# Kernel tuning notes

Hardware: AMD Instinct MI355X
Metric: run time of the kernel (lower is better)

## Reference

```python
import jax, jax.numpy as jnp
import numpy as np

N = 2048       # num nodes
E = 4096       # num edges
D_NODE = 128
D_EDGE = 128
H = 4          # heads
DH = D_EDGE // H
C = 16         # num classes
NODE_K = N // 2   # node_k_ratio = 0.5
EDGE_K = E // 2   # edge_k_ratio = 0.5
NEG = -1e9


def setup_inputs() -> dict:
    key = jax.random.key(0)
    ks = jax.random.split(key, 16)
    w = lambda k, shape: jax.random.normal(k, shape, jnp.float32) * 0.02
    return {
        "node_features": jax.random.normal(ks[0], (N, D_NODE), jnp.float32),
        "edge_features": jax.random.normal(ks[1], (E, D_EDGE), jnp.float32),
        "edge_index": jax.random.randint(ks[2], (2, E), 0, N, jnp.int32),
        # ImportanceRouter: scalar scores per node / edge
        "w_router_n": w(ks[3], (D_NODE,)),
        "w_router_e": w(ks[4], (D_EDGE,)),
        # EdgeAttention projections
        "w_e": w(ks[5], (D_EDGE, D_EDGE)),
        "w_n": w(ks[6], (D_NODE, D_EDGE)),
        "w_q": w(ks[7], (D_EDGE, D_EDGE)),
        "w_k": w(ks[8], (D_EDGE, D_EDGE)),
        "w_v": w(ks[9], (D_EDGE, D_EDGE)),
        "w_o": w(ks[10], (D_EDGE, D_EDGE)),
        # classifier MLP: Linear -> GELU -> Linear
        "w1": w(ks[11], (D_EDGE, D_EDGE)),
        "b1": jnp.zeros((D_EDGE,), jnp.float32),
        "w2": w(ks[12], (D_EDGE, C)),
        "b2": jnp.zeros((C,), jnp.float32),
    }


def reference(node_features, edge_features, edge_index,
              w_router_n, w_router_e,
              w_e, w_n, w_q, w_k, w_v, w_o,
              w1, b1, w2, b2):
    src, dst = edge_index[0], edge_index[1]

    # --- ImportanceRouter: node/edge scores ---
    ns = node_features @ w_router_n   # [N]
    es = edge_features @ w_router_e   # [E]

    # --- apply_top_k(node_k_ratio=0.5, edge_k_ratio=0.5) ---
    _, nidx = jax.lax.top_k(ns, NODE_K)
    node_mask = jnp.zeros((N,), bool).at[nidx].set(True)
    _, eidx = jax.lax.top_k(es, EDGE_K)
    edge_topk = jnp.zeros((E,), bool).at[eidx].set(True)
    edge_mask = edge_topk & node_mask[src] & node_mask[dst]   # [E]

    ef = edge_features * edge_mask[:, None].astype(edge_features.dtype)

    # --- build_edge_adjacency: edges sharing a node attend to each other ---
    adj = ((src[:, None] == src[None, :]) | (src[:, None] == dst[None, :]) |
           (dst[:, None] == src[None, :]) | (dst[:, None] == dst[None, :]))  # [E,E]

    # --- EdgeAttention: edge rep mixes edge feats and endpoint node feats ---
    h = ef @ w_e + (node_features[src] + node_features[dst]) @ w_n   # [E, D_EDGE]
    q = (h @ w_q).reshape(E, H, DH)
    k = (h @ w_k).reshape(E, H, DH)
    v = (h @ w_v).reshape(E, H, DH)
    scores = jnp.einsum('ehd,fhd->hef', q, k) / np.float32(np.sqrt(DH))  # [H,E,E]
    scores = jnp.where(adj[None, :, :], scores, NEG)
    attn = jax.nn.softmax(scores, axis=-1)
    o = jnp.einsum('hef,fhd->ehd', attn, v).reshape(E, D_EDGE) @ w_o    # [E, D_EDGE]

    # --- classifier: Linear -> GELU -> Linear ---
    x = jax.nn.gelu(o @ w1 + b1)
    logits = x @ w2 + b2            # [E, C]
    return logits
```

## Files before the change

### kernel.cpp

```cpp
#include <hip/hip_runtime.h>
#include <hip/hip_bf16.h>
#include <math.h>

#define NN 2048
#define NE 4096
#define D 128
#define NODE_K 1024
#define EDGE_K 2048
#define CAP 64

typedef const __hip_bfloat16* bfp;
typedef unsigned short u16;
typedef __attribute__((ext_vector_type(8))) short short8;
typedef __attribute__((ext_vector_type(4))) float floatx4;

#define MFMA16(a, b, c) __builtin_amdgcn_mfma_f32_16x16x32_bf16(a, b, c, 0, 0, 0)

__device__ __forceinline__ float b2f(__hip_bfloat16 x) { return __bfloat162float(x); }

__device__ __forceinline__ float ldx(const void* p, size_t i, int f) {
  return f ? ((const float*)p)[i] : b2f(((bfp)p)[i]);
}
__device__ __forceinline__ float4 ldx4(const void* p, size_t i4, int f) {
  if (f) return ((const float4*)p)[i4];
  ushort4 u = ((const ushort4*)p)[i4];
  float4 r;
  r.x = __uint_as_float(((unsigned)u.x) << 16);
  r.y = __uint_as_float(((unsigned)u.y) << 16);
  r.z = __uint_as_float(((unsigned)u.z) << 16);
  r.w = __uint_as_float(((unsigned)u.w) << 16);
  return r;
}

__device__ __forceinline__ void split2(float x, u16& hi, u16& lo) {
  unsigned u = __float_as_uint(x);
  unsigned h = (u + 0x7FFFu + ((u >> 16) & 1u)) >> 16;
  hi = (u16)h;
  float r = x - __uint_as_float(h << 16);
  unsigned v = __float_as_uint(r);
  lo = (u16)((v + 0x7FFFu + ((v >> 16) & 1u)) >> 16);
}
__device__ __forceinline__ void build_frags(const float* v8, short8& fh, short8& fl) {
  #pragma unroll
  for (int i = 0; i < 8; ++i) {
    u16 h, l;
    split2(v8[i], h, l);
    fh[i] = (short)h; fl[i] = (short)l;
  }
}

__device__ __forceinline__ int detect_f(const u16* raw, int* s4) {
  int t = threadIdx.x;
  int weird = 0;
  for (int i = t; i < 1024; i += blockDim.x) {
    unsigned int bits = ((unsigned int)raw[i]) << 16;
    float x = __uint_as_float(bits);
    float ax = fabsf(x);
    if (!(ax <= 1e3f) || (x != 0.f && ax < 1e-12f)) weird++;
  }
  #pragma unroll
  for (int m = 32; m >= 1; m >>= 1) weird += __shfl_xor(weird, m);
  int nw = (int)blockDim.x >> 6;
  if ((t & 63) == 0) s4[t >> 6] = weird;
  __syncthreads();
  int tot = 0;
  for (int i = 0; i < nw; ++i) tot += s4[i];
  return (tot > 50) ? 1 : 0;
}

struct K1Args {
  const void *nf, *ef, *wrn, *wre;
  const void* w[7];
  float *ns, *es;
  int *deg, *flag;
  u16 *wtHi, *wtLo;
  u16 *feHi, *feLo;
};

#define SCORE_BLOCKS ((NN + NE) / 4)
#define WPREP_BLOCKS 112
#define FSPLIT_BLOCKS 192
__global__ __launch_bounds__(256) void scores_prep_kernel(K1Args a) {
  __shared__ int s4[4];
  int b = blockIdx.x, t = threadIdx.x;
  int f = detect_f((const u16*)a.nf, s4);
  if (b < SCORE_BLOCKS) {
    int wid = b * 4 + (t >> 6), lane = t & 63;
    const void* base; const void* w; float* out; size_t r0;
    if (wid < NN) { base = a.nf; r0 = (size_t)wid * D; w = a.wrn; out = a.ns + wid; }
    else { int r = wid - NN; base = a.ef; r0 = (size_t)r * D; w = a.wre; out = a.es + r; }
    double p = (double)ldx(base, r0 + lane, f) * (double)ldx(w, lane, f)
             + (double)ldx(base, r0 + lane + 64, f) * (double)ldx(w, lane + 64, f);
    #pragma unroll
    for (int m = 32; m >= 1; m >>= 1) p += __shfl_xor(p, m);
    if (lane == 0) *out = (float)p;
  } else if (b == SCORE_BLOCKS) {
    if (t == 0) a.flag[0] = f;
    for (int i = t; i < NN; i += 256) a.deg[i] = 0;
  } else if (b <= SCORE_BLOCKS + WPREP_BLOCKS) {
    int tau = (b - SCORE_BLOCKS - 1) * 256 + t;
    int w = tau >> 12, rem = tau & 4095;
    int n = rem >> 5, k0 = (rem & 31) * 4;
    ushort4 hi, lo;
    split2(ldx(a.w[w], (size_t)(k0 + 0) * 128 + n, f), hi.x, lo.x);
    split2(ldx(a.w[w], (size_t)(k0 + 1) * 128 + n, f), hi.y, lo.y);
    split2(ldx(a.w[w], (size_t)(k0 + 2) * 128 + n, f), hi.z, lo.z);
    split2(ldx(a.w[w], (size_t)(k0 + 3) * 128 + n, f), hi.w, lo.w);
    ((ushort4*)a.wtHi)[tau] = hi;
    ((ushort4*)a.wtLo)[tau] = lo;
  } else {
    int fb = b - SCORE_BLOCKS - 1 - WPREP_BLOCKS;
    #pragma unroll
    for (int i = 0; i < 4; ++i) {
      int g4 = fb * 1024 + i * 256 + t;
      float4 x = (g4 < NN * D / 4) ? ldx4(a.nf, g4, f)
                                   : ldx4(a.ef, g4 - NN * D / 4, f);
      ushort4 hi, lo;
      split2(x.x, hi.x, lo.x);
      split2(x.y, hi.y, lo.y);
      split2(x.z, hi.z, lo.z);
      split2(x.w, hi.w, lo.w);
      ((ushort4*)a.feHi)[g4] = hi;
      ((ushort4*)a.feLo)[g4] = lo;
    }
  }
}

#define NMB (NN / 4)
#define EMB (NE / 4)
__global__ __launch_bounds__(256) void mask_lists_kernel(
    const float* __restrict__ ns, const float* __restrict__ es,
    const int* __restrict__ src, const int* __restrict__ dst,
    int* __restrict__ node_mask, int* __restrict__ edge_topk,
    int* __restrict__ deg, int* __restrict__ lists) {
  __shared__ float s[NE];
  int b = blockIdx.x, t = threadIdx.x;
  if (b < NMB) {
    for (int i = t; i < NN; i += 256) s[i] = ns[i];
    __syncthreads();
    int i = b * 4 + (t >> 6), lane = t & 63;
    float si = s[i];
    int rank = 0;
    for (int j = lane; j < NN; j += 64) {
      float sj = s[j];
      rank += (sj > si) || (sj == si && j < i);
    }
    #pragma unroll
    for (int m = 32; m >= 1; m >>= 1) rank += __shfl_xor(rank, m);
    if (lane == 0) node_mask[i] = (rank < NODE_K) ? 1 : 0;
  } else if (b < NMB + EMB) {
    for (int i = t; i < NE; i += 256) s[i] = es[i];
    __syncthreads();
    int i = (b - NMB) * 4 + (t >> 6), lane = t & 63;
    float si = s[i];
    int rank = 0;
    for (int j = lane; j < NE; j += 64) {
      float sj = s[j];
      rank += (sj > si) || (sj == si && j < i);
    }
    #pragma unroll
    for (int m = 32; m >= 1; m >>= 1) rank += __shfl_xor(rank, m);
    if (lane == 0) edge_topk[i] = (rank < EDGE_K) ? 1 : 0;
  } else {
    int e = (b - NMB - EMB) * 256 + t;
    if (e < NE) {
      int sn = src[e], dn = dst[e];
      int p = atomicAdd(&deg[sn], 1);
      if (p >= 0 && p < CAP) lists[sn * CAP + p] = e;
      if (dn != sn) {
        p = atomicAdd(&deg[dn], 1);
        if (p >= 0 && p < CAP) lists[dn * CAP + p] = e;
      }
    }
  }
}

__global__ __launch_bounds__(512) void h_qkv_mfma_kernel(
    const u16* __restrict__ feHi, const u16* __restrict__ feLo,
    const int* __restrict__ src, const int* __restrict__ dst,
    const int* __restrict__ node_mask, const int* __restrict__ edge_topk,
    const u16* __restrict__ wtHi, const u16* __restrict__ wtLo,
    float* __restrict__ qkv) {
  __shared__ __align__(16) float hf[8 * 64 * 4];
  int t = threadIdx.x;
  int wave = t >> 6, lane = t & 63;
  int qd = lane >> 4, c = lane & 15;
  int row0 = blockIdx.x * 16;
  int e = row0 + c;
  int sn = src[e], dn = dst[e];
  bool em = edge_topk[e] && node_mask[sn] && node_mask[dn];
  int n0 = wave * 16;
  const u16* efH = feHi + (size_t)NN * D;
  const u16* efL = feLo + (size_t)NN * D;
  const short8 z8 = {0, 0, 0, 0, 0, 0, 0, 0};

  short8 A1h[4], A1l[4], Sh[4], Sl[4], Dh[4], Dl[4];
  short8 BEh[4], BEl[4], BNh[4], BNl[4];
  #pragma unroll
  for (int ks = 0; ks < 4; ++ks) {
    int k0 = ks * 32 + qd * 8;
    A1h[ks] = *(const short8*)(efH + (size_t)e * D + k0);
    A1l[ks] = *(const short8*)(efL + (size_t)e * D + k0);
    Sh[ks]  = *(const short8*)(feHi + (size_t)sn * D + k0);
    Sl[ks]  = *(const short8*)(feLo + (size_t)sn * D + k0);
    Dh[ks]  = *(const short8*)(feHi + (size_t)dn * D + k0);
    Dl[ks]  = *(const short8*)(feLo + (size_t)dn * D + k0);
    size_t bo = (size_t)(n0 + c) * 128 + k0;
    BEh[ks] = *(const short8*)(wtHi + bo);
    BEl[ks] = *(const short8*)(wtLo + bo);
    BNh[ks] = *(const short8*)(wtHi + 16384 + bo);
    BNl[ks] = *(const short8*)(wtLo + 16384 + bo);
  }
  if (!em) {
    #pragma unroll
    for (int ks = 0; ks < 4; ++ks) { A1h[ks] = z8; A1l[ks] = z8; }
  }
  floatx4 accE = {0.f, 0.f, 0.f, 0.f};
  floatx4 accN = {0.f, 0.f, 0.f, 0.f};
  #pragma unroll
  for (int ks = 0; ks < 4; ++ks) {
    accE = MFMA16(A1h[ks], BEh[ks], accE);
    accN = MFMA16(Sh[ks], BNh[ks], accN);
    accE = MFMA16(A1l[ks], BEh[ks], accE);
    accN = MFMA16(Sl[ks], BNh[ks], accN);
    accE = MFMA16(A1h[ks], BEl[ks], accE);
    accN = MFMA16(Sh[ks], BNl[ks], accN);
    accN = MFMA16(Dh[ks], BNh[ks], accN);
    accN = MFMA16(Dl[ks], BNh[ks], accN);
    accN = MFMA16(Dh[ks], BNl[ks], accN);
  }
  {
    int np = n0 + c;
    int kd = np >> 5, qq = (np >> 3) & 3, half = (c >> 2) & 1, j4 = c & 3;
    #pragma unroll
    for (int r = 0; r < 4; ++r)
      hf[((kd * 2 + half) * 64 + qq * 16 + 4 * qd + r) * 4 + j4] = accE[r] + accN[r];
  }
  short8 BQh[4], BQl[4], BKh[4], BKl[4], BVh[4], BVl[4];
  #pragma unroll
  for (int ks = 0; ks < 4; ++ks) {
    size_t bo = (size_t)(n0 + c) * 128 + ks * 32 + qd * 8;
    BQh[ks] = *(const short8*)(wtHi + 2 * 16384 + bo);
    BQl[ks] = *(const short8*)(wtLo + 2 * 16384 + bo);
    BKh[ks] = *(const short8*)(wtHi + 3 * 16384 + bo);
    BKl[ks] = *(const short8*)(wtLo + 3 * 16384 + bo);
    BVh[ks] = *(const short8*)(wtHi + 4 * 16384 + bo);
    BVl[ks] = *(const short8*)(wtLo + 4 * 16384 + bo);
  }
  __syncthreads();
  floatx4 aq = {0.f, 0.f, 0.f, 0.f};
  floatx4 ak = {0.f, 0.f, 0.f, 0.f};
  floatx4 av = {0.f, 0.f, 0.f, 0.f};
  #pragma unroll
  for (int ks = 0; ks < 4; ++ks) {
    float4 p0 = *(const float4*)&hf[((ks * 2 + 0) * 64 + lane) * 4];
    float4 p1 = *(const float4*)&hf[((ks * 2 + 1) * 64 + lane) * 4];
    float v8[8] = {p0.x, p0.y, p0.z, p0.w, p1.x, p1.y, p1.z, p1.w};
    short8 ah, al;
    build_frags(v8, ah, al);
    aq = MFMA16(ah, BQh[ks], aq);
    ak = MFMA16(ah, BKh[ks], ak);
    av = MFMA16(ah, BVh[ks], av);
    aq = MFMA16(al, BQh[ks], aq);
    ak = MFMA16(al, BKh[ks], ak);
    av = MFMA16(al, BVh[ks], av);
    aq = MFMA16(ah, BQl[ks], aq);
    ak = MFMA16(ah, BKl[ks], ak);
    av = MFMA16(ah, BVl[ks], av);
  }
  #pragma unroll
  for (int r = 0; r < 4; ++r) {
    size_t ro = (size_t)(row0 + 4 * qd + r) * D + n0 + c;
    qkv[ro] = aq[r];
    qkv[(size_t)NE * D + ro] = ak[r];
    qkv[(size_t)2 * NE * D + ro] = av[r];
  }
}

__global__ void attn_kernel(const float* __restrict__ q, const float* __restrict__ k,
                            const float* __restrict__ v, const int* __restrict__ src,
                            const int* __restrict__ dst, const int* __restrict__ deg,
                            const int* __restrict__ lists, float* __restrict__ ao) {
  int e = blockIdx.x;
  int j = threadIdx.x;
  float qj = q[(size_t)e * D + j];
  int sn = src[e], dn = dst[e];
  float m = -1e30f, l = 0.f, acc = 0.f;
  const float scale = 0.17677669529663687f;
  int degA = max(0, min(deg[sn], CAP));
  for (int i = 0; i < degA; ++i) {
    int fe = lists[sn * CAP + i];
    float p = qj * k[(size_t)fe * D + j];
    p += __shfl_xor(p, 16); p += __shfl_xor(p, 8); p += __shfl_xor(p, 4);
    p += __shfl_xor(p, 2);  p += __shfl_xor(p, 1);
    float s = p * scale;
    float vj = v[(size_t)fe * D + j];
    float mn = fmaxf(m, s);
    float corr = expf(m - mn);
    float w = expf(s - mn);
    l = l * corr + w;
    acc = acc * corr + w * vj;
    m = mn;
  }
  if (dn != sn) {
    int degB = max(0, min(deg[dn], CAP));
    for (int i = 0; i < degB; ++i) {
      int fe = lists[dn * CAP + i];
      if (src[fe] == sn || dst[fe] == sn) continue;
      float p = qj * k[(size_t)fe * D + j];
      p += __shfl_xor(p, 16); p += __shfl_xor(p, 8); p += __shfl_xor(p, 4);
      p += __shfl_xor(p, 2);  p += __shfl_xor(p, 1);
      float s = p * scale;
      float vj = v[(size_t)fe * D + j];
      float mn = fmaxf(m, s);
      float corr = expf(m - mn);
      float w = expf(s - mn);
      l = l * corr + w;
      acc = acc * corr + w * vj;
      m = mn;
    }
  }
  ao[(size_t)e * D + j] = acc / fmaxf(l, 1e-37f);
}

__global__ __launch_bounds__(512) void o_mlp_mfma_kernel(
    const float* __restrict__ ao,
    const u16* __restrict__ wtHi, const u16* __restrict__ wtLo,
    const void* __restrict__ b1, const void* __restrict__ w2,
    const void* __restrict__ b2, const int* __restrict__ flag,
    void* __restrict__ out) {
  __shared__ __align__(16) float hf[8 * 64 * 4];
  __shared__ float xl[16 * 132];
  __shared__ float w2l[128 * 16];
  int t = threadIdx.x;
  int wave = t >> 6, lane = t & 63;
  int qd = lane >> 4, c = lane & 15;
  int f = flag[0];
  int row0 = blockIdx.x * 16;
  int n0 = wave * 16;

  short8 BOh[4], BOl[4], B1h[4], B1l[4];
  #pragma unroll
  for (int ks = 0; ks < 4; ++ks) {
    size_t bo = (size_t)(n0 + c) * 128 + ks * 32 + qd * 8;
    BOh[ks] = *(const short8*)(wtHi + 5 * 16384 + bo);
    BOl[ks] = *(const short8*)(wtLo + 5 * 16384 + bo);
    B1h[ks] = *(const short8*)(wtHi + 6 * 16384 + bo);
    B1l[ks] = *(const short8*)(wtLo + 6 * 16384 + bo);
  }
  floatx4 acc = {0.f, 0.f, 0.f, 0.f};
  #pragma unroll
  for (int ks = 0; ks < 4; ++ks) {
    int k0 = ks * 32 + qd * 8;
    const float* ap = ao + (size_t)(row0 + c) * D + k0;
    float4 p0 = *(const float4*)ap;
    float4 p1 = *(const float4*)(ap + 4);
    float v8[8] = {p0.x, p0.y, p0.z, p0.w, p1.x, p1.y, p1.z, p1.w};
    short8 ah, al;
    build_frags(v8, ah, al);
    acc = MFMA16(ah, BOh[ks], acc);
    acc = MFMA16(al, BOh[ks], acc);
    acc = MFMA16(ah, BOl[ks], acc);
  }
  {
    int np = n0 + c;
    int kd = np >> 5, qq = (np >> 3) & 3, half = (c >> 2) & 1, j4 = c & 3;
    #pragma unroll
    for (int r = 0; r < 4; ++r)
      hf[((kd * 2 + half) * 64 + qq * 16 + 4 * qd + r) * 4 + j4] = acc[r];
  }
  __syncthreads();
  floatx4 a2c = {0.f, 0.f, 0.f, 0.f};
  #pragma unroll
  for (int ks = 0; ks < 4; ++ks) {
    float4 p0 = *(const float4*)&hf[((ks * 2 + 0) * 64 + lane) * 4];
    float4 p1 = *(const float4*)&hf[((ks * 2 + 1) * 64 + lane) * 4];
    float v8[8] = {p0.x, p0.y, p0.z, p0.w, p1.x, p1.y, p1.z, p1.w};
    short8 ah, al;
    build_frags(v8, ah, al);
    a2c = MFMA16(ah, B1h[ks], a2c);
    a2c = MFMA16(al, B1h[ks], a2c);
    a2c = MFMA16(ah, B1l[ks], a2c);
  }
  float bj = ldx(b1, n0 + c, f);
  #pragma unroll
  for (int r = 0; r < 4; ++r) {
    float u = a2c[r] + bj;
    float inner = 0.7978845608028654f * (u + 0.044715f * u * u * u);
    xl[(4 * qd + r) * 132 + n0 + c] = 0.5f * u * (1.f + tanhf(inner));
  }
  for (int i = t; i < D * 16; i += 512) w2l[i] = ldx(w2, i, f);
  __syncthreads();
  if (t < 256) {
    int r = t >> 4, cc = t & 15;
    float s = 0.f;
    for (int kk = 0; kk < D; ++kk) s += xl[r * 132 + kk] * w2l[kk * 16 + cc];
    s += ldx(b2, cc, f);
    int idx = (row0 + r) * 16 + cc;
    if (f) ((float*)out)[idx] = s;
    else ((__hip_bfloat16*)out)[idx] = __float2bfloat16(s);
  }
}

extern "C" void kernel_launch(void* const* d_in, const int* in_sizes, int n_in,
                              void* d_out, int out_size, void* d_ws, size_t ws_size,
                              hipStream_t stream) {
  const int* eidx = (const int*)d_in[2];
  const int* src = eidx;
  const int* dst = eidx + NE;

  size_t off = 0;
  char* base = (char*)d_ws;
  auto alloc = [&](size_t nbytes) -> void* {
    void* p = base + off;
    off += (nbytes + 255) & ~(size_t)255;
    return p;
  };
  int* flag      = (int*)alloc(256);
  float* ns      = (float*)alloc(NN * sizeof(float));
  float* es      = (float*)alloc(NE * sizeof(float));
  int* node_mask = (int*)alloc(NN * sizeof(int));
  int* edge_topk = (int*)alloc(NE * sizeof(int));
  int* deg       = (int*)alloc(NN * sizeof(int));
  int* lists     = (int*)alloc((size_t)NN * CAP * sizeof(int));
  u16* wtHi      = (u16*)alloc((size_t)7 * 16384 * sizeof(u16));
  u16* wtLo      = (u16*)alloc((size_t)7 * 16384 * sizeof(u16));
  u16* feHi      = (u16*)alloc((size_t)(NN + NE) * D * sizeof(u16));
  u16* feLo      = (u16*)alloc((size_t)(NN + NE) * D * sizeof(u16));
  float* qkv     = (float*)alloc((size_t)3 * NE * D * sizeof(float));
  float* ao      = (float*)alloc((size_t)NE * D * sizeof(float));
  float* qb = qkv, *kb = qkv + NE * D, *vb = qkv + 2 * NE * D;

  K1Args a1;
  a1.nf = d_in[0]; a1.ef = d_in[1]; a1.wrn = d_in[3]; a1.wre = d_in[4];
  a1.w[0] = d_in[5];  a1.w[1] = d_in[6];  a1.w[2] = d_in[7];
  a1.w[3] = d_in[8];  a1.w[4] = d_in[9];  a1.w[5] = d_in[10]; a1.w[6] = d_in[11];
  a1.ns = ns; a1.es = es; a1.deg = deg; a1.flag = flag;
  a1.wtHi = wtHi; a1.wtLo = wtLo; a1.feHi = feHi; a1.feLo = feLo;

  scores_prep_kernel<<<SCORE_BLOCKS + 1 + WPREP_BLOCKS + FSPLIT_BLOCKS, 256, 0,
                       stream>>>(a1);
  mask_lists_kernel<<<NMB + EMB + NE / 256, 256, 0, stream>>>(
      ns, es, src, dst, node_mask, edge_topk, deg, lists);
  h_qkv_mfma_kernel<<<NE / 16, 512, 0, stream>>>(
      feHi, feLo, src, dst, node_mask, edge_topk, wtHi, wtLo, qkv);
  attn_kernel<<<NE, 128, 0, stream>>>(qb, kb, vb, src, dst, deg, lists, ao);
  o_mlp_mfma_kernel<<<NE / 16, 512, 0, stream>>>(
      ao, wtHi, wtLo, d_in[12], d_in[13], d_in[14], flag, d_out);
}
```

Baseline: 139.1 us.

## Halve rows per block in MFMA kernels and batch top-k ranks per wave

The h/qkv and o/MLP MFMA kernels now process 8 edges per block instead of 16. Half of each 16-row MFMA tile is zero-padded, which doubles the block count to spread work across more CUs at the cost of wasted MFMA work and duplicated weight loads. Weight fragments are now loaded inside the k-loop instead of being preloaded into register arrays, which lowers register pressure. The top-k rank kernel now has each wave rank 4 elements, so far fewer blocks each reload the score array into shared memory.

```diff
diff --git a/kernel.cpp b/kernel.cpp
--- a/kernel.cpp
+++ b/kernel.cpp
@@ -126,8 +126,8 @@
   }
 }
 
-#define NMB (NN / 4)
-#define EMB (NE / 4)
+#define NMB (NN / 16)
+#define EMB (NE / 16)
 __global__ __launch_bounds__(256) void mask_lists_kernel(
     const float* __restrict__ ns, const float* __restrict__ es,
     const int* __restrict__ src, const int* __restrict__ dst,
@@ -135,32 +135,39 @@
     int* __restrict__ deg, int* __restrict__ lists) {
   __shared__ float s[NE];
   int b = blockIdx.x, t = threadIdx.x;
+  int wave = t >> 6, lane = t & 63;
   if (b < NMB) {
     for (int i = t; i < NN; i += 256) s[i] = ns[i];
     __syncthreads();
-    int i = b * 4 + (t >> 6), lane = t & 63;
-    float si = s[i];
-    int rank = 0;
-    for (int j = lane; j < NN; j += 64) {
-      float sj = s[j];
-      rank += (sj > si) || (sj == si && j < i);
-    }
-    #pragma unroll
-    for (int m = 32; m >= 1; m >>= 1) rank += __shfl_xor(rank, m);
-    if (lane == 0) node_mask[i] = (rank < NODE_K) ? 1 : 0;
+    #pragma unroll
+    for (int ti = 0; ti < 4; ++ti) {
+      int i = b * 16 + wave * 4 + ti;
+      float si = s[i];
+      int rank = 0;
+      for (int j = lane; j < NN; j += 64) {
+        float sj = s[j];
+        rank += (sj > si) || (sj == si && j < i);
+      }
+      #pragma unroll
+      for (int m = 32; m >= 1; m >>= 1) rank += __shfl_xor(rank, m);
+      if (lane == 0) node_mask[i] = (rank < NODE_K) ? 1 : 0;
+    }
   } else if (b < NMB + EMB) {
     for (int i = t; i < NE; i += 256) s[i] = es[i];
     __syncthreads();
-    int i = (b - NMB) * 4 + (t >> 6), lane = t & 63;
-    float si = s[i];
-    int rank = 0;
-    for (int j = lane; j < NE; j += 64) {
-      float sj = s[j];
-      rank += (sj > si) || (sj == si && j < i);
-    }
-    #pragma unroll
-    for (int m = 32; m >= 1; m >>= 1) rank += __shfl_xor(rank, m);
-    if (lane == 0) edge_topk[i] = (rank < EDGE_K) ? 1 : 0;
+    #pragma unroll
+    for (int ti = 0; ti < 4; ++ti) {
+      int i = (b - NMB) * 16 + wave * 4 + ti;
+      float si = s[i];
+      int rank = 0;
+      for (int j = lane; j < NE; j += 64) {
+        float sj = s[j];
+        rank += (sj > si) || (sj == si && j < i);
+      }
+      #pragma unroll
+      for (int m = 32; m >= 1; m >>= 1) rank += __shfl_xor(rank, m);
+      if (lane == 0) edge_topk[i] = (rank < EDGE_K) ? 1 : 0;
+    }
   } else {
     int e = (b - NMB - EMB) * 256 + t;
     if (e < NE) {
@@ -185,17 +192,17 @@
   int t = threadIdx.x;
   int wave = t >> 6, lane = t & 63;
   int qd = lane >> 4, c = lane & 15;
-  int row0 = blockIdx.x * 16;
-  int e = row0 + c;
+  int row0 = blockIdx.x * 8;
+  bool valid = c < 8;
+  int e = row0 + (valid ? c : 0);
   int sn = src[e], dn = dst[e];
-  bool em = edge_topk[e] && node_mask[sn] && node_mask[dn];
+  bool em = valid && edge_topk[e] && node_mask[sn] && node_mask[dn];
   int n0 = wave * 16;
   const u16* efH = feHi + (size_t)NN * D;
   const u16* efL = feLo + (size_t)NN * D;
   const short8 z8 = {0, 0, 0, 0, 0, 0, 0, 0};
 
   short8 A1h[4], A1l[4], Sh[4], Sl[4], Dh[4], Dl[4];
-  short8 BEh[4], BEl[4], BNh[4], BNl[4];
   #pragma unroll
   for (int ks = 0; ks < 4; ++ks) {
     int k0 = ks * 32 + qd * 8;
@@ -205,29 +212,33 @@
     Sl[ks]  = *(const short8*)(feLo + (size_t)sn * D + k0);
     Dh[ks]  = *(const short8*)(feHi + (size_t)dn * D + k0);
     Dl[ks]  = *(const short8*)(feLo + (size_t)dn * D + k0);
-    size_t bo = (size_t)(n0 + c) * 128 + k0;
-    BEh[ks] = *(const short8*)(wtHi + bo);
-    BEl[ks] = *(const short8*)(wtLo + bo);
-    BNh[ks] = *(const short8*)(wtHi + 16384 + bo);
-    BNl[ks] = *(const short8*)(wtLo + 16384 + bo);
   }
   if (!em) {
     #pragma unroll
     for (int ks = 0; ks < 4; ++ks) { A1h[ks] = z8; A1l[ks] = z8; }
+  }
+  if (!valid) {
+    #pragma unroll
+    for (int ks = 0; ks < 4; ++ks) { Sh[ks] = z8; Sl[ks] = z8; Dh[ks] = z8; Dl[ks] = z8; }
   }
   floatx4 accE = {0.f, 0.f, 0.f, 0.f};
   floatx4 accN = {0.f, 0.f, 0.f, 0.f};
   #pragma unroll
   for (int ks = 0; ks < 4; ++ks) {
-    accE = MFMA16(A1h[ks], BEh[ks], accE);
-    accN = MFMA16(Sh[ks], BNh[ks], accN);
-    accE = MFMA16(A1l[ks], BEh[ks], accE);
-    accN = MFMA16(Sl[ks], BNh[ks], accN);
-    accE = MFMA16(A1h[ks], BEl[ks], accE);
-    accN = MFMA16(Sh[ks], BNl[ks], accN);
-    accN = MFMA16(Dh[ks], BNh[ks], accN);
-    accN = MFMA16(Dl[ks], BNh[ks], accN);
-    accN = MFMA16(Dh[ks], BNl[ks], accN);
+    size_t bo = (size_t)(n0 + c) * 128 + ks * 32 + qd * 8;
+    short8 bEh = *(const short8*)(wtHi + bo);
+    short8 bEl = *(const short8*)(wtLo + bo);
+    short8 bNh = *(const short8*)(wtHi + 16384 + bo);
+    short8 bNl = *(const short8*)(wtLo + 16384 + bo);
+    accE = MFMA16(A1h[ks], bEh, accE);
+    accN = MFMA16(Sh[ks], bNh, accN);
+    accE = MFMA16(A1l[ks], bEh, accE);
+    accN = MFMA16(Sl[ks], bNh, accN);
+    accE = MFMA16(A1h[ks], bEl, accE);
+    accN = MFMA16(Sh[ks], bNl, accN);
+    accN = MFMA16(Dh[ks], bNh, accN);
+    accN = MFMA16(Dl[ks], bNh, accN);
+    accN = MFMA16(Dh[ks], bNl, accN);
   }
   {
     int np = n0 + c;
@@ -235,17 +246,6 @@
     #pragma unroll
     for (int r = 0; r < 4; ++r)
       hf[((kd * 2 + half) * 64 + qq * 16 + 4 * qd + r) * 4 + j4] = accE[r] + accN[r];
-  }
-  short8 BQh[4], BQl[4], BKh[4], BKl[4], BVh[4], BVl[4];
-  #pragma unroll
-  for (int ks = 0; ks < 4; ++ks) {
-    size_t bo = (size_t)(n0 + c) * 128 + ks * 32 + qd * 8;
-    BQh[ks] = *(const short8*)(wtHi + 2 * 16384 + bo);
-    BQl[ks] = *(const short8*)(wtLo + 2 * 16384 + bo);
-    BKh[ks] = *(const short8*)(wtHi + 3 * 16384 + bo);
-    BKl[ks] = *(const short8*)(wtLo + 3 * 16384 + bo);
-    BVh[ks] = *(const short8*)(wtHi + 4 * 16384 + bo);
-    BVl[ks] = *(const short8*)(wtLo + 4 * 16384 + bo);
   }
   __syncthreads();
   floatx4 aq = {0.f, 0.f, 0.f, 0.f};
@@ -258,22 +258,31 @@
     float v8[8] = {p0.x, p0.y, p0.z, p0.w, p1.x, p1.y, p1.z, p1.w};
     short8 ah, al;
     build_frags(v8, ah, al);
-    aq = MFMA16(ah, BQh[ks], aq);
-    ak = MFMA16(ah, BKh[ks], ak);
-    av = MFMA16(ah, BVh[ks], av);
-    aq = MFMA16(al, BQh[ks], aq);
-    ak = MFMA16(al, BKh[ks], ak);
-    av = MFMA16(al, BVh[ks], av);
-    aq = MFMA16(ah, BQl[ks], aq);
-    ak = MFMA16(ah, BKl[ks], ak);
-    av = MFMA16(ah, BVl[ks], av);
-  }
-  #pragma unroll
-  for (int r = 0; r < 4; ++r) {
-    size_t ro = (size_t)(row0 + 4 * qd + r) * D + n0 + c;
-    qkv[ro] = aq[r];
-    qkv[(size_t)NE * D + ro] = ak[r];
-    qkv[(size_t)2 * NE * D + ro] = av[r];
+    size_t bo = (size_t)(n0 + c) * 128 + ks * 32 + qd * 8;
+    short8 BQh = *(const short8*)(wtHi + 2 * 16384 + bo);
+    short8 BKh = *(const short8*)(wtHi + 3 * 16384 + bo);
+    short8 BVh = *(const short8*)(wtHi + 4 * 16384 + bo);
+    short8 BQl = *(const short8*)(wtLo + 2 * 16384 + bo);
+    short8 BKl = *(const short8*)(wtLo + 3 * 16384 + bo);
+    short8 BVl = *(const short8*)(wtLo + 4 * 16384 + bo);
+    aq = MFMA16(ah, BQh, aq);
+    ak = MFMA16(ah, BKh, ak);
+    av = MFMA16(ah, BVh, av);
+    aq = MFMA16(al, BQh, aq);
+    ak = MFMA16(al, BKh, ak);
+    av = MFMA16(al, BVh, av);
+    aq = MFMA16(ah, BQl, aq);
+    ak = MFMA16(ah, BKl, ak);
+    av = MFMA16(ah, BVl, av);
+  }
+  if (qd < 2) {
+    #pragma unroll
+    for (int r = 0; r < 4; ++r) {
+      size_t ro = (size_t)(row0 + 4 * qd + r) * D + n0 + c;
+      qkv[ro] = aq[r];
+      qkv[(size_t)NE * D + ro] = ak[r];
+      qkv[(size_t)2 * NE * D + ro] = av[r];
+    }
   }
 }
 
@@ -330,37 +339,40 @@
     const void* __restrict__ b2, const int* __restrict__ flag,
     void* __restrict__ out) {
   __shared__ __align__(16) float hf[8 * 64 * 4];
-  __shared__ float xl[16 * 132];
+  __shared__ float xl[8 * 132];
   __shared__ float w2l[128 * 16];
   int t = threadIdx.x;
   int wave = t >> 6, lane = t & 63;
   int qd = lane >> 4, c = lane & 15;
   int f = flag[0];
-  int row0 = blockIdx.x * 16;
+  int row0 = blockIdx.x * 8;
+  bool valid = c < 8;
   int n0 = wave * 16;
-
-  short8 BOh[4], BOl[4], B1h[4], B1l[4];
-  #pragma unroll
-  for (int ks = 0; ks < 4; ++ks) {
-    size_t bo = (size_t)(n0 + c) * 128 + ks * 32 + qd * 8;
-    BOh[ks] = *(const short8*)(wtHi + 5 * 16384 + bo);
-    BOl[ks] = *(const short8*)(wtLo + 5 * 16384 + bo);
-    B1h[ks] = *(const short8*)(wtHi + 6 * 16384 + bo);
-    B1l[ks] = *(const short8*)(wtLo + 6 * 16384 + bo);
-  }
+  const float zero8[8] = {0, 0, 0, 0, 0, 0, 0, 0};
+
   floatx4 acc = {0.f, 0.f, 0.f, 0.f};
   #pragma unroll
   for (int ks = 0; ks < 4; ++ks) {
     int k0 = ks * 32 + qd * 8;
-    const float* ap = ao + (size_t)(row0 + c) * D + k0;
-    float4 p0 = *(const float4*)ap;
-    float4 p1 = *(const float4*)(ap + 4);
-    float v8[8] = {p0.x, p0.y, p0.z, p0.w, p1.x, p1.y, p1.z, p1.w};
+    float v8[8];
+    if (valid) {
+      const float* ap = ao + (size_t)(row0 + c) * D + k0;
+      float4 p0 = *(const float4*)ap;
+      float4 p1 = *(const float4*)(ap + 4);
+      v8[0] = p0.x; v8[1] = p0.y; v8[2] = p0.z; v8[3] = p0.w;
+      v8[4] = p1.x; v8[5] = p1.y; v8[6] = p1.z; v8[7] = p1.w;
+    } else {
+      #pragma unroll
+      for (int i = 0; i < 8; ++i) v8[i] = zero8[i];
+    }
     short8 ah, al;
     build_frags(v8, ah, al);
-    acc = MFMA16(ah, BOh[ks], acc);
-    acc = MFMA16(al, BOh[ks], acc);
-    acc = MFMA16(ah, BOl[ks], acc);
+    size_t bo = (size_t)(n0 + c) * 128 + k0;
+    short8 bh = *(const short8*)(wtHi + 5 * 16384 + bo);
+    short8 bl = *(const short8*)(wtLo + 5 * 16384 + bo);
+    acc = MFMA16(ah, bh, acc);
+    acc = MFMA16(al, bh, acc);
+    acc = MFMA16(ah, bl, acc);
   }
   {
     int np = n0 + c;
@@ -378,20 +390,25 @@
     float v8[8] = {p0.x, p0.y, p0.z, p0.w, p1.x, p1.y, p1.z, p1.w};
     short8 ah, al;
     build_frags(v8, ah, al);
-    a2c = MFMA16(ah, B1h[ks], a2c);
-    a2c = MFMA16(al, B1h[ks], a2c);
-    a2c = MFMA16(ah, B1l[ks], a2c);
+    size_t bo = (size_t)(n0 + c) * 128 + ks * 32 + qd * 8;
+    short8 bh = *(const short8*)(wtHi + 6 * 16384 + bo);
+    short8 bl = *(const short8*)(wtLo + 6 * 16384 + bo);
+    a2c = MFMA16(ah, bh, a2c);
+    a2c = MFMA16(al, bh, a2c);
+    a2c = MFMA16(ah, bl, a2c);
   }
   float bj = ldx(b1, n0 + c, f);
-  #pragma unroll
-  for (int r = 0; r < 4; ++r) {
-    float u = a2c[r] + bj;
-    float inner = 0.7978845608028654f * (u + 0.044715f * u * u * u);
-    xl[(4 * qd + r) * 132 + n0 + c] = 0.5f * u * (1.f + tanhf(inner));
+  if (qd < 2) {
+    #pragma unroll
+    for (int r = 0; r < 4; ++r) {
+      float u = a2c[r] + bj;
+      float inner = 0.7978845608028654f * (u + 0.044715f * u * u * u);
+      xl[(4 * qd + r) * 132 + n0 + c] = 0.5f * u * (1.f + tanhf(inner));
+    }
   }
   for (int i = t; i < D * 16; i += 512) w2l[i] = ldx(w2, i, f);
   __syncthreads();
-  if (t < 256) {
+  if (t < 128) {
     int r = t >> 4, cc = t & 15;
     float s = 0.f;
     for (int kk = 0; kk < D; ++kk) s += xl[r * 132 + kk] * w2l[kk * 16 + cc];
@@ -442,9 +459,9 @@
                        stream>>>(a1);
   mask_lists_kernel<<<NMB + EMB + NE / 256, 256, 0, stream>>>(
       ns, es, src, dst, node_mask, edge_topk, deg, lists);
-  h_qkv_mfma_kernel<<<NE / 16, 512, 0, stream>>>(
+  h_qkv_mfma_kernel<<<NE / 8, 512, 0, stream>>>(
       feHi, feLo, src, dst, node_mask, edge_topk, wtHi, wtLo, qkv);
   attn_kernel<<<NE, 128, 0, stream>>>(qb, kb, vb, src, dst, deg, lists, ao);
-  o_mlp_mfma_kernel<<<NE / 16, 512, 0, stream>>>(
+  o_mlp_mfma_kernel<<<NE / 8, 512, 0, stream>>>(
       ao, wtHi, wtLo, d_in[12], d_in[13], d_in[14], flag, d_out);
 }
```

New measurement: 158.3 us. 13.8% more time.
